# Performance work log

Measured on AMD Instinct MI355X. Metric: run time of the kernel, lower is better.

## Reference

```python
import jax, jax.numpy as jnp
import numpy as np

B = 4          # per_gpu_batch_size
P = 16         # n_contexts
N = B * P      # fused passage dim = 64
L = 512        # seq_len
H = 768        # hidden_size
S = 16         # sentence spans per passage


def setup_inputs() -> dict:
    key = jax.random.key(0)
    k1, k2, k3 = jax.random.split(key, 3)
    hidden_states = jax.random.normal(k1, (N, L, H), jnp.float32)
    # nn.Linear weight [out, in]; original init std=1.0 saturates tanh, use 0.02 scale for sane numerics
    dense_w = jax.random.normal(k2, (H, H), jnp.float32) * 0.02
    dense_b = jnp.zeros((H,), jnp.float32)
    attention_mask = jnp.ones((N, L), jnp.int32)
    # strictly increasing boundaries -> S non-empty, ragged, contiguous spans per passage
    r = jnp.sort(jax.random.randint(k3, (N, S + 1), 0, L - S), axis=-1) + jnp.arange(S + 1, dtype=jnp.int32)
    spans = jnp.stack([r[:, :-1], r[:, 1:]], axis=-1).astype(jnp.int32)  # [N, S, 2]
    return dict(hidden_states=hidden_states, dense_w=dense_w, dense_b=dense_b,
                attention_mask=attention_mask, spans=spans)


def reference(hidden_states, dense_w, dense_b, attention_mask, spans):
    # sentence_spans branch: token_tensor = hidden_states (all tokens)
    # pooled_output = activation(dense(token_tensor)); cls_norm_type == 'none' -> no norm
    pooled = jnp.tanh(jnp.einsum('nlh,oh->nlo', hidden_states, dense_w) + dense_b)  # [N, L, H]
    pooled_output_passages = pooled[:, 0]  # [N, H]
    # ragged per-span mean pooling, vectorized as a masked segment reduce
    pos = jnp.arange(L, dtype=jnp.int32)                         # [L]
    start = spans[..., 0][..., None]                             # [N, S, 1]
    end = spans[..., 1][..., None]                               # [N, S, 1]
    m = ((pos >= start) & (pos < end)).astype(pooled.dtype)      # [N, S, L]
    sums = jnp.einsum('nsl,nlh->nsh', m, pooled)                 # [N, S, H]
    counts = (spans[..., 1] - spans[..., 0]).astype(pooled.dtype)[..., None]  # [N, S, 1]
    sentence_embeddings = (sums / counts).reshape(N * S, H)      # [N*S, H]
    # all S spans valid per passage -> mask of zeros (0 = valid in original code)
    sentence_mask = jnp.zeros((N, S), jnp.float32)
    return pooled_output_passages, sentence_embeddings, sentence_mask
```

## Files before the change

kernel.cpp:

```cpp
#include <hip/hip_runtime.h>
#include <hip/hip_bf16.h>

#define NPASS 64
#define LSEQ  512
#define HDIM  768
#define NSPAN 16
#define MTOT  (NPASS*LSEQ)
#define OFF_SENT (NPASS*HDIM)
#define W_ELEMS (HDIM*HDIM)

#define BM 128
#define BN 128
#define BK 32
#define NK (HDIM/BK)

typedef __bf16 bf16x8 __attribute__((ext_vector_type(8)));
typedef __bf16 bf16x4 __attribute__((ext_vector_type(4)));
typedef float  f32x4  __attribute__((ext_vector_type(4)));

__device__ inline unsigned short f2bf(float f) {
  __hip_bfloat16 h = __float2bfloat16(f);
  unsigned short u; __builtin_memcpy(&u, &h, 2); return u;
}

__device__ inline float fast_tanh(float x) {
  const float ax = fabsf(x);
  const float t  = __expf(-2.0f * ax);
  const float r  = (1.0f - t) * __builtin_amdgcn_rcpf(1.0f + t);
  return copysignf(r, x);
}

__device__ inline bf16x8 cvt8(f32x4 lo, f32x4 hi) {
  union { bf16x4 h[2]; bf16x8 v; } u;
  u.h[0] = __builtin_convertvector(lo, bf16x4);
  u.h[1] = __builtin_convertvector(hi, bf16x4);
  return u.v;
}

__global__ __launch_bounds__(256) void convert_w_kernel(
    const float* __restrict__ W, unsigned short* __restrict__ Wb)
{
  const int i = (blockIdx.x * 256 + threadIdx.x) * 8;
  const float4 a = *(const float4*)(W + i);
  const float4 b = *(const float4*)(W + i + 4);
  union { unsigned short us[8]; uint4 v; } o;
  o.us[0]=f2bf(a.x); o.us[1]=f2bf(a.y); o.us[2]=f2bf(a.z); o.us[3]=f2bf(a.w);
  o.us[4]=f2bf(b.x); o.us[5]=f2bf(b.y); o.us[6]=f2bf(b.z); o.us[7]=f2bf(b.w);
  *(uint4*)(Wb + i) = o.v;
}

__global__ __launch_bounds__(256) void gemm_fused_kernel(
    const float* __restrict__ A,
    const unsigned short* __restrict__ Wb,
    const float* __restrict__ bias,
    const int* __restrict__ spans,
    float* __restrict__ out)
{
  __shared__ __align__(16) float          As[2][BM*BK];
  __shared__ __align__(16) unsigned short Bs[2][BN*BK];
  __shared__ int   sp_st[NSPAN], sp_en[NSPAN];
  __shared__ float inv_s[NSPAN];
  __shared__ short sid_l[BM];
  __shared__ float bias_s[BN];

  const int tid  = threadIdx.x;
  const int wave = tid >> 6;
  const int lane = tid & 63;
  const int quad = lane >> 4;
  const int lr   = lane & 15;
  const int wm   = wave >> 1;
  const int wn   = wave & 1;
  const int tile_m = blockIdx.x * BM;
  const int tile_n = blockIdx.y * BN;
  const int npass  = tile_m >> 9;
  const int l0     = tile_m & 511;

  auto stage = [&](int k, int buf) {
    const int k0 = k * BK;
    #pragma unroll
    for (int j = 0; j < 6; ++j) {
      const int seg = j * 4 + wave;
      if (seg < 16) {
        const int row = seg * 8 + (lane >> 3);
        const int gs  = (lane & 7) ^ ((lane >> 3) & 7);
        const float* g = A + (size_t)(tile_m + row) * HDIM + (k0 + gs * 4);
        __builtin_amdgcn_global_load_lds(
            (const __attribute__((address_space(1))) void*)g,
            (__attribute__((address_space(3))) void*)(As[buf] + seg * 256),
            16, 0, 0);
      } else {
        const int s2  = seg - 16;
        const int row = s2 * 16 + (lane >> 2);
        const int gs  = (lane & 3) ^ ((lane >> 3) & 3);
        const unsigned short* g =
            Wb + (size_t)(tile_n + row) * HDIM + (k0 + gs * 8);
        __builtin_amdgcn_global_load_lds(
            (const __attribute__((address_space(1))) void*)g,
            (__attribute__((address_space(3))) void*)(Bs[buf] + s2 * 512),
            16, 0, 0);
      }
    }
  };

  stage(0, 0);
  if (tid < NSPAN) {
    const int st = spans[(npass * NSPAN + tid) * 2 + 0];
    const int en = spans[(npass * NSPAN + tid) * 2 + 1];
    sp_st[tid] = st; sp_en[tid] = en; inv_s[tid] = 1.0f / (float)(en - st);
  }
  if (tid >= 128 && tid < 128 + BN) bias_s[tid - 128] = bias[tile_n + tid - 128];
  __syncthreads();
  if (tid < BM) {
    const int l = l0 + tid;
    short s = -1;
    #pragma unroll
    for (int i = 0; i < NSPAN; ++i)
      if (l >= sp_st[i] && l < sp_en[i]) s = (short)i;
    sid_l[tid] = s;
  }

  f32x4 acc[4][4];
  #pragma unroll
  for (int i = 0; i < 4; ++i)
    #pragma unroll
    for (int j = 0; j < 4; ++j)
      acc[i][j] = (f32x4){0.f, 0.f, 0.f, 0.f};

  for (int k = 0; k < NK; ++k) {
    const int cur = k & 1;
    if (k + 1 < NK) stage(k + 1, cur ^ 1);

    bf16x8 af[4], bfr[4];
    #pragma unroll
    for (int mt = 0; mt < 4; ++mt) {
      const int r  = wm * 64 + mt * 16 + lr;
      const int sw = r & 7;
      const float* base = As[cur] + r * BK;
      const f32x4 lo = *(const f32x4*)(base + (((quad * 2    ) ^ sw) * 4));
      const f32x4 hi = *(const f32x4*)(base + (((quad * 2 + 1) ^ sw) * 4));
      af[mt] = cvt8(lo, hi);
    }
    #pragma unroll
    for (int nt = 0; nt < 4; ++nt) {
      const int r = wn * 64 + nt * 16 + lr;
      const int g = quad ^ ((r >> 1) & 3);
      bfr[nt] = *(const bf16x8*)(Bs[cur] + (r * BK + g * 8));
    }

    #pragma unroll
    for (int mt = 0; mt < 4; ++mt)
      #pragma unroll
      for (int nt = 0; nt < 4; ++nt)
        acc[mt][nt] = __builtin_amdgcn_mfma_f32_16x16x32_bf16(
            af[mt], bfr[nt], acc[mt][nt], 0, 0, 0);

    __syncthreads();
  }

  #pragma unroll
  for (int nt = 0; nt < 4; ++nt) {
    const int lcolo = wn * 64 + nt * 16 + lr;
    const int col   = tile_n + lcolo;
    const float bv  = bias_s[lcolo];
    float* sent_col = out + OFF_SENT + (size_t)(npass * NSPAN) * HDIM + col;
    #pragma unroll
    for (int mt = 0; mt < 4; ++mt) {
      const int rowbase = wm * 64 + mt * 16 + quad * 4;
      int prev = -1; float run = 0.f;
      #pragma unroll
      for (int r = 0; r < 4; ++r) {
        const int lrw = rowbase + r;
        const float v = fast_tanh(acc[mt][nt][r] + bv);
        if (l0 == 0 && lrw == 0) out[(size_t)npass * HDIM + col] = v;
        const int s = sid_l[lrw];
        if (s != prev) {
          if (prev >= 0) unsafeAtomicAdd(sent_col + (size_t)prev * HDIM, run * inv_s[prev]);
          prev = s; run = 0.f;
        }
        run += v;
      }
      if (prev >= 0) unsafeAtomicAdd(sent_col + (size_t)prev * HDIM, run * inv_s[prev]);
    }
  }
}

extern "C" void kernel_launch(void* const* d_in, const int* in_sizes, int n_in,
                              void* d_out, int out_size, void* d_ws, size_t ws_size,
                              hipStream_t stream) {
  const float* hs  = (const float*)d_in[0];
  const float* w   = (const float*)d_in[1];
  const float* bsc = (const float*)d_in[2];
  const int* spans = (const int*)d_in[4];
  float* out = (float*)d_out;

  unsigned short* Wb = (unsigned short*)d_ws;

  hipMemsetAsync(d_out, 0, (size_t)out_size * sizeof(float), stream);

  convert_w_kernel<<<dim3(W_ELEMS / 8 / 256), dim3(256), 0, stream>>>(w, Wb);

  dim3 grid(MTOT / BM, HDIM / BN);
  gemm_fused_kernel<<<grid, dim3(256), 0, stream>>>(hs, Wb, bsc, spans, out);
}
```

Baseline: 269.7 us.

## Fuse weight conversion into single kernel with per-passage blocks and LDS span reduction

Replaces the memset, weight-convert and tiled GEMM kernels with one kernel. Each 512-thread block handles a whole passage (512 rows) against a 96-column weight slice, converted to bf16 straight into LDS. The activation tile streams from global into registers with no LDS double-buffering or per-step barriers. Span sums accumulate in LDS and are written once, which removes global atomics and the output memset. Block indices are remapped so blocks sharing a passage land on the same XCD. In exchange, each block re-converts its fp32 weight slice, uses about 144KB of LDS, and the A loads are per-lane strided global reads with no LDS staging.

```diff
diff --git a/kernel.cpp b/kernel.cpp
--- a/kernel.cpp
+++ b/kernel.cpp
@@ -5,23 +5,20 @@
 #define LSEQ  512
 #define HDIM  768
 #define NSPAN 16
-#define MTOT  (NPASS*LSEQ)
 #define OFF_SENT (NPASS*HDIM)
-#define W_ELEMS (HDIM*HDIM)
+#define OFF_MASK (OFF_SENT + NPASS*NSPAN*HDIM)
 
-#define BM 128
-#define BN 128
-#define BK 32
-#define NK (HDIM/BK)
+#define BN   96
+#define NTN  6
+#define BK   32
+#define NK   (HDIM/BK)
+#define NTILES (HDIM/BN)
+#define NBLK (NPASS*NTILES)
+#define THREADS 512
 
 typedef __bf16 bf16x8 __attribute__((ext_vector_type(8)));
 typedef __bf16 bf16x4 __attribute__((ext_vector_type(4)));
 typedef float  f32x4  __attribute__((ext_vector_type(4)));
-
-__device__ inline unsigned short f2bf(float f) {
-  __hip_bfloat16 h = __float2bfloat16(f);
-  unsigned short u; __builtin_memcpy(&u, &h, 2); return u;
-}
 
 __device__ inline float fast_tanh(float x) {
   const float ax = fabsf(x);
@@ -37,151 +34,147 @@
   return u.v;
 }
 
-__global__ __launch_bounds__(256) void convert_w_kernel(
-    const float* __restrict__ W, unsigned short* __restrict__ Wb)
-{
-  const int i = (blockIdx.x * 256 + threadIdx.x) * 8;
-  const float4 a = *(const float4*)(W + i);
-  const float4 b = *(const float4*)(W + i + 4);
-  union { unsigned short us[8]; uint4 v; } o;
-  o.us[0]=f2bf(a.x); o.us[1]=f2bf(a.y); o.us[2]=f2bf(a.z); o.us[3]=f2bf(a.w);
-  o.us[4]=f2bf(b.x); o.us[5]=f2bf(b.y); o.us[6]=f2bf(b.z); o.us[7]=f2bf(b.w);
-  *(uint4*)(Wb + i) = o.v;
-}
-
-__global__ __launch_bounds__(256) void gemm_fused_kernel(
+__global__ __launch_bounds__(THREADS, 2) void fused_kernel(
     const float* __restrict__ A,
-    const unsigned short* __restrict__ Wb,
+    const float* __restrict__ W,
     const float* __restrict__ bias,
-    const int* __restrict__ spans,
+    const int*   __restrict__ spans,
     float* __restrict__ out)
 {
-  __shared__ __align__(16) float          As[2][BM*BK];
-  __shared__ __align__(16) unsigned short Bs[2][BN*BK];
-  __shared__ int   sp_st[NSPAN], sp_en[NSPAN];
+  __shared__ __align__(16) unsigned short Wl[BN * HDIM];
+  __shared__ float sent_lds[NSPAN][BN];
   __shared__ float inv_s[NSPAN];
-  __shared__ short sid_l[BM];
   __shared__ float bias_s[BN];
+  __shared__ short sid_l[LSEQ];
 
-  const int tid  = threadIdx.x;
+  const int tid = threadIdx.x;
+  const int b   = blockIdx.x;
+  const int xcd = b & 7;
+  const int t   = b >> 3;
+  const int p   = ((t >> 3) << 3) | xcd;
+  const int ntb = t & 7;
+  const int tile_n = ntb * BN;
+
+
+  {
+    const float* Wp = W + (size_t)tile_n * HDIM;
+    #pragma unroll
+    for (int j = 0; j < (BN * (HDIM / 8)) / THREADS; ++j) {
+      const int g  = j * THREADS + tid;
+      const int wr = g / (HDIM / 8);
+      const int kg = g % (HDIM / 8);
+      const float* src = Wp + (size_t)wr * HDIM + kg * 8;
+      const f32x4 lo = *(const f32x4*)src;
+      const f32x4 hi = *(const f32x4*)(src + 4);
+      const int kgs = kg ^ (wr & 7);
+      *(bf16x8*)(Wl + (size_t)wr * HDIM + kgs * 8) = cvt8(lo, hi);
+    }
+  }
+
+  {
+    int st[NSPAN], en[NSPAN];
+    #pragma unroll
+    for (int i = 0; i < NSPAN; ++i) {
+      st[i] = spans[(p * NSPAN + i) * 2 + 0];
+      en[i] = spans[(p * NSPAN + i) * 2 + 1];
+    }
+    short s = -1;
+    #pragma unroll
+    for (int i = 0; i < NSPAN; ++i)
+      if (tid >= st[i] && tid < en[i]) s = (short)i;
+    sid_l[tid] = s;
+  }
+  if (tid < NSPAN)
+    inv_s[tid] = 1.0f / (float)(spans[(p * NSPAN + tid) * 2 + 1] -
+                                spans[(p * NSPAN + tid) * 2 + 0]);
+  if (tid < BN) bias_s[tid] = bias[tile_n + tid];
+  for (int i = tid; i < NSPAN * BN; i += THREADS) (&sent_lds[0][0])[i] = 0.f;
+
+  __syncthreads();
+
   const int wave = tid >> 6;
   const int lane = tid & 63;
   const int quad = lane >> 4;
   const int lr   = lane & 15;
-  const int wm   = wave >> 1;
-  const int wn   = wave & 1;
-  const int tile_m = blockIdx.x * BM;
-  const int tile_n = blockIdx.y * BN;
-  const int npass  = tile_m >> 9;
-  const int l0     = tile_m & 511;
 
-  auto stage = [&](int k, int buf) {
-    const int k0 = k * BK;
+  const float* Ab = A + ((size_t)p * LSEQ + wave * 64 + lr) * HDIM + quad * 8;
+
+  f32x4 acc[4][NTN];
+  #pragma unroll
+  for (int mt = 0; mt < 4; ++mt)
     #pragma unroll
-    for (int j = 0; j < 6; ++j) {
-      const int seg = j * 4 + wave;
-      if (seg < 16) {
-        const int row = seg * 8 + (lane >> 3);
-        const int gs  = (lane & 7) ^ ((lane >> 3) & 7);
-        const float* g = A + (size_t)(tile_m + row) * HDIM + (k0 + gs * 4);
-        __builtin_amdgcn_global_load_lds(
-            (const __attribute__((address_space(1))) void*)g,
-            (__attribute__((address_space(3))) void*)(As[buf] + seg * 256),
-            16, 0, 0);
-      } else {
-        const int s2  = seg - 16;
-        const int row = s2 * 16 + (lane >> 2);
-        const int gs  = (lane & 3) ^ ((lane >> 3) & 3);
-        const unsigned short* g =
-            Wb + (size_t)(tile_n + row) * HDIM + (k0 + gs * 8);
-        __builtin_amdgcn_global_load_lds(
-            (const __attribute__((address_space(1))) void*)g,
-            (__attribute__((address_space(3))) void*)(Bs[buf] + s2 * 512),
-            16, 0, 0);
+    for (int nt = 0; nt < NTN; ++nt)
+      acc[mt][nt] = (f32x4){0.f, 0.f, 0.f, 0.f};
+
+  f32x4 alo[4], ahi[4];
+  #pragma unroll
+  for (int mt = 0; mt < 4; ++mt) {
+    const float* s0 = Ab + (size_t)mt * 16 * HDIM;
+    alo[mt] = *(const f32x4*)s0;
+    ahi[mt] = *(const f32x4*)(s0 + 4);
+  }
+
+  #pragma unroll
+  for (int k = 0; k < NK; ++k) {
+    bf16x8 wf[NTN];
+    #pragma unroll
+    for (int nt = 0; nt < NTN; ++nt) {
+      const int wr = nt * 16 + lr;
+      const int kg = (4 * k + quad) ^ (lr & 7);
+      wf[nt] = *(const bf16x8*)(Wl + (size_t)wr * HDIM + kg * 8);
+    }
+    bf16x8 abf[4];
+    #pragma unroll
+    for (int mt = 0; mt < 4; ++mt) abf[mt] = cvt8(alo[mt], ahi[mt]);
+    if (k + 1 < NK) {
+      #pragma unroll
+      for (int mt = 0; mt < 4; ++mt) {
+        const float* s1 = Ab + (size_t)mt * 16 * HDIM + (k + 1) * BK;
+        alo[mt] = *(const f32x4*)s1;
+        ahi[mt] = *(const f32x4*)(s1 + 4);
       }
     }
-  };
-
-  stage(0, 0);
-  if (tid < NSPAN) {
-    const int st = spans[(npass * NSPAN + tid) * 2 + 0];
-    const int en = spans[(npass * NSPAN + tid) * 2 + 1];
-    sp_st[tid] = st; sp_en[tid] = en; inv_s[tid] = 1.0f / (float)(en - st);
-  }
-  if (tid >= 128 && tid < 128 + BN) bias_s[tid - 128] = bias[tile_n + tid - 128];
-  __syncthreads();
-  if (tid < BM) {
-    const int l = l0 + tid;
-    short s = -1;
-    #pragma unroll
-    for (int i = 0; i < NSPAN; ++i)
-      if (l >= sp_st[i] && l < sp_en[i]) s = (short)i;
-    sid_l[tid] = s;
-  }
-
-  f32x4 acc[4][4];
-  #pragma unroll
-  for (int i = 0; i < 4; ++i)
-    #pragma unroll
-    for (int j = 0; j < 4; ++j)
-      acc[i][j] = (f32x4){0.f, 0.f, 0.f, 0.f};
-
-  for (int k = 0; k < NK; ++k) {
-    const int cur = k & 1;
-    if (k + 1 < NK) stage(k + 1, cur ^ 1);
-
-    bf16x8 af[4], bfr[4];
-    #pragma unroll
-    for (int mt = 0; mt < 4; ++mt) {
-      const int r  = wm * 64 + mt * 16 + lr;
-      const int sw = r & 7;
-      const float* base = As[cur] + r * BK;
-      const f32x4 lo = *(const f32x4*)(base + (((quad * 2    ) ^ sw) * 4));
-      const f32x4 hi = *(const f32x4*)(base + (((quad * 2 + 1) ^ sw) * 4));
-      af[mt] = cvt8(lo, hi);
-    }
-    #pragma unroll
-    for (int nt = 0; nt < 4; ++nt) {
-      const int r = wn * 64 + nt * 16 + lr;
-      const int g = quad ^ ((r >> 1) & 3);
-      bfr[nt] = *(const bf16x8*)(Bs[cur] + (r * BK + g * 8));
-    }
-
+    __builtin_amdgcn_s_setprio(1);
     #pragma unroll
     for (int mt = 0; mt < 4; ++mt)
       #pragma unroll
-      for (int nt = 0; nt < 4; ++nt)
+      for (int nt = 0; nt < NTN; ++nt)
         acc[mt][nt] = __builtin_amdgcn_mfma_f32_16x16x32_bf16(
-            af[mt], bfr[nt], acc[mt][nt], 0, 0, 0);
-
-    __syncthreads();
+            abf[mt], wf[nt], acc[mt][nt], 0, 0, 0);
+    __builtin_amdgcn_s_setprio(0);
   }
 
   #pragma unroll
-  for (int nt = 0; nt < 4; ++nt) {
-    const int lcolo = wn * 64 + nt * 16 + lr;
-    const int col   = tile_n + lcolo;
-    const float bv  = bias_s[lcolo];
-    float* sent_col = out + OFF_SENT + (size_t)(npass * NSPAN) * HDIM + col;
+  for (int nt = 0; nt < NTN; ++nt) {
+    const int col = nt * 16 + lr;
+    const float bv = bias_s[col];
     #pragma unroll
     for (int mt = 0; mt < 4; ++mt) {
-      const int rowbase = wm * 64 + mt * 16 + quad * 4;
+      const int rowbase = wave * 64 + mt * 16 + quad * 4;
       int prev = -1; float run = 0.f;
       #pragma unroll
       for (int r = 0; r < 4; ++r) {
-        const int lrw = rowbase + r;
+        const int row = rowbase + r;
         const float v = fast_tanh(acc[mt][nt][r] + bv);
-        if (l0 == 0 && lrw == 0) out[(size_t)npass * HDIM + col] = v;
-        const int s = sid_l[lrw];
+        if (row == 0) out[(size_t)p * HDIM + tile_n + col] = v;
+        const int s = sid_l[row];
         if (s != prev) {
-          if (prev >= 0) unsafeAtomicAdd(sent_col + (size_t)prev * HDIM, run * inv_s[prev]);
+          if (prev >= 0) atomicAdd(&sent_lds[prev][col], run);
           prev = s; run = 0.f;
         }
         run += v;
       }
-      if (prev >= 0) unsafeAtomicAdd(sent_col + (size_t)prev * HDIM, run * inv_s[prev]);
+      if (prev >= 0) atomicAdd(&sent_lds[prev][col], run);
     }
   }
+  __syncthreads();
+
+  for (int i = tid; i < NSPAN * BN; i += THREADS) {
+    const int s = i / BN, c = i % BN;
+    out[OFF_SENT + ((size_t)p * NSPAN + s) * HDIM + tile_n + c] =
+        sent_lds[s][c] * inv_s[s];
+  }
+  if (ntb == 0 && tid < NSPAN) out[OFF_MASK + p * NSPAN + tid] = 0.f;
 }
 
 extern "C" void kernel_launch(void* const* d_in, const int* in_sizes, int n_in,
@@ -191,14 +184,7 @@
   const float* w   = (const float*)d_in[1];
   const float* bsc = (const float*)d_in[2];
   const int* spans = (const int*)d_in[4];
-  float* out = (float*)d_out;
 
-  unsigned short* Wb = (unsigned short*)d_ws;
-
-  hipMemsetAsync(d_out, 0, (size_t)out_size * sizeof(float), stream);
-
-  convert_w_kernel<<<dim3(W_ELEMS / 8 / 256), dim3(256), 0, stream>>>(w, Wb);
-
-  dim3 grid(MTOT / BM, HDIM / BN);
-  gemm_fused_kernel<<<grid, dim3(256), 0, stream>>>(hs, Wb, bsc, spans, out);
+  fused_kernel<<<dim3(NBLK), dim3(THREADS), 0, stream>>>(
+      hs, w, bsc, spans, (float*)d_out);
 }
```

Measured after the change: 241.9 us. 1.11x faster.
